# Kernel tuning notes

Hardware: AMD Instinct MI355X
Metric: run time of the kernel (lower is better)

## Reference

```python
import jax, jax.numpy as jnp
import numpy as np
from jax import lax

B, D, E, H, W = 256, 64, 16, 64, 64
PROJ, FC, NA = 512, 1024, 2

def _conv(x, w, pad):
    # x: [N,C,H,W], w: [O,I,kh,kw]
    return lax.conv_general_dilated(x, w, (1, 1), [(pad, pad), (pad, pad)],
                                    dimension_numbers=('NCHW', 'OIHW', 'NCHW'))

def _maxpool2(x):
    return lax.reduce_window(x, -jnp.inf, lax.max, (1, 1, 2, 2), (1, 1, 2, 2), 'VALID')

def _sample_conv(x, w, b):
    # per-sample conv with its own gathered expert weights: x [D,h,w], w [D,D,3,3]
    y = lax.conv_general_dilated(x[None], w, (1, 1), [(1, 1), (1, 1)],
                                 dimension_numbers=('NCHW', 'OIHW', 'NCHW'))[0]
    return y + b[:, None, None]

_expert_conv = jax.vmap(_sample_conv)  # batch of samples, each with its own kernel

def setup_inputs() -> dict:
    key = jax.random.key(0)
    ks = jax.random.split(key, 12)
    s = 0.05
    return {
        'image': jax.random.normal(ks[0], (B, 3, H, W), jnp.float32),
        'question': jax.random.randint(ks[1], (B, 8), 0, E),
        'stem_w0': jax.random.normal(ks[2], (D, 3, 3, 3), jnp.float32) * s,
        'stem_b0': jnp.zeros((D,), jnp.float32),
        'stem_w': jax.random.normal(ks[3], (3, D, D, 3, 3), jnp.float32) * s,
        'stem_b': jnp.zeros((3, D), jnp.float32),
        'exp_w1': jax.random.normal(ks[4], (E, D, D, 3, 3), jnp.float32) * s,
        'exp_b1': jnp.zeros((E, D), jnp.float32),
        'exp_w2': jax.random.normal(ks[5], (E, D, D, 3, 3), jnp.float32) * s,
        'exp_b2': jnp.zeros((E, D), jnp.float32),
        'proj_w': jax.random.normal(ks[6], (PROJ, D, 1, 1), jnp.float32) * s,
        'proj_b': jnp.zeros((PROJ,), jnp.float32),
        'fc1_w': jax.random.normal(ks[7], (FC, PROJ * 8 * 8), jnp.float32) * 0.01,
        'fc1_b': jnp.zeros((FC,), jnp.float32),
        'fc2_w': jax.random.normal(ks[8], (NA, FC), jnp.float32) * 0.01,
        'fc2_b': jnp.zeros((NA,), jnp.float32),
    }

def reference(image, question, stem_w0, stem_b0, stem_w, stem_b,
              exp_w1, exp_b1, exp_w2, exp_b2,
              proj_w, proj_b, fc1_w, fc1_b, fc2_w, fc2_b):
    # --- stem: 4 conv3x3 + ReLU, maxpool after layers 0 and 2 (64->32->16) ---
    h = jax.nn.relu(_conv(image, stem_w0, 1) + stem_b0[None, :, None, None])
    h = _maxpool2(h)
    h = jax.nn.relu(_conv(h, stem_w[0], 1) + stem_b[0][None, :, None, None])
    h = jax.nn.relu(_conv(h, stem_w[1], 1) + stem_b[1][None, :, None, None])
    h = _maxpool2(h)
    h = jax.nn.relu(_conv(h, stem_w[2], 1) + stem_b[2][None, :, None, None])
    # --- chain1 routing: cols (lhs=4, rel=5, rhs=7) each pick a ResidualBlock expert ---
    for col in (4, 5, 7):
        idx = question[:, col]                       # [B] expert ids
        w1, b1 = exp_w1[idx], exp_b1[idx]            # gather per-sample kernels
        w2, b2 = exp_w2[idx], exp_b2[idx]
        mid = jax.nn.relu(_expert_conv(h, w1, b1))   # conv1 + ReLU
        out = _expert_conv(mid, w2, b2)              # conv2 (no BN)
        h = jax.nn.relu(h + out)                     # residual + ReLU
    # --- classifier: 1x1 proj + ReLU, maxpool2, flatten, fc, fc ---
    c = jax.nn.relu(_conv(h, proj_w, 0) + proj_b[None, :, None, None])  # [B,512,16,16]
    c = _maxpool2(c)                                                     # [B,512,8,8]
    c = c.reshape(c.shape[0], -1)                                        # [B,32768]
    c = jax.nn.relu(c @ fc1_w.T + fc1_b)
    return c @ fc2_w.T + fc2_b                                           # [B,2]
```

## Files before the change

kernel.cpp:

```cpp
#include <hip/hip_runtime.h>
#include <cstddef>


typedef _Float16 half8 __attribute__((ext_vector_type(8)));
typedef _Float16 half4_t __attribute__((ext_vector_type(4)));
typedef float f32x4 __attribute__((ext_vector_type(4)));

#define LO_SCALE 2048.0f
#define LO_INV (1.0f / 2048.0f)

__global__ void wxform_k(const float* __restrict__ src, _Float16* __restrict__ dst,
                         int nlayers) {
    int id = blockIdx.x * 256 + threadIdx.x;
    if (id >= nlayers * 36864) return;
    int layer = id / 36864, idx = id % 36864;
    int j = idx & 7, l = (idx >> 3) & 63, nt = (idx >> 9) & 3;
    int icc = (idx >> 11) & 1, tap = idx >> 12;
    int kl = (l >> 4) * 8 + j, ic = icc * 32 + kl, oc = nt * 16 + (l & 15);
    float v = src[(size_t)layer * 36864 + (oc * 64 + ic) * 9 + tap];
    _Float16 hi = (_Float16)v;
    _Float16 lo = (_Float16)((v - (float)hi) * LO_SCALE);
    dst[(size_t)layer * 73728 + idx] = hi;
    dst[(size_t)layer * 73728 + 36864 + idx] = lo;
}

__global__ void pwxform_k(const float* __restrict__ src, _Float16* __restrict__ dst) {
    int id = blockIdx.x * 256 + threadIdx.x;
    if (id >= 32768) return;
    int j = id & 7, l = (id >> 3) & 63, icc = (id >> 9) & 1, nt = id >> 10;
    int kl = (l >> 4) * 8 + j, ic = icc * 32 + kl, oc = nt * 16 + (l & 15);
    float v = src[oc * 64 + ic];
    _Float16 hi = (_Float16)v;
    _Float16 lo = (_Float16)((v - (float)hi) * LO_SCALE);
    dst[id] = hi;
    dst[32768 + id] = lo;
}

__global__ void c1wx_k(const float* __restrict__ src, _Float16* __restrict__ dst) {
    int id = blockIdx.x * 256 + threadIdx.x;
    if (id >= 2048) return;
    int j = id & 7, l = (id >> 3) & 63, nt = id >> 9;
    int k = (l >> 4) * 8 + j, oc = nt * 16 + (l & 15);
    float v = 0.f;
    if (k < 27) {
        int ic = k / 9, tap = k % 9;
        v = src[(oc * 3 + ic) * 9 + tap];
    }
    _Float16 hi = (_Float16)v;
    _Float16 lo = (_Float16)((v - (float)hi) * LO_SCALE);
    dst[id] = hi;
    dst[2048 + id] = lo;
}

__global__ __launch_bounds__(256, 2)
void conv1m_k(const float* __restrict__ img, const _Float16* __restrict__ wf,
              const float* __restrict__ b0, _Float16* __restrict__ out) {
    const size_t NE1 = 16777216;
    int b = blockIdx.x, t = blockIdx.y;
    int ty0 = (t >> 2) * 8, tx0 = (t & 3) * 16;
    __shared__ float halo[3][10][18];
    __shared__ __align__(16) _Float16 lin[2 * 5120];

    int tid = threadIdx.x, lane = tid & 63, wv = tid >> 6;
    const float* imb = img + (size_t)b * 3 * 64 * 64;
    for (int i = tid; i < 540; i += 256) {
        int c = i / 180, rem = i % 180, r = rem / 18, cc = rem % 18;
        int gy = ty0 - 1 + r, gx = tx0 - 1 + cc;
        float v = 0.f;
        if (gy >= 0 && gy < 64 && gx >= 0 && gx < 64) v = imb[(c * 64 + gy) * 64 + gx];
        halo[c][r][cc] = v;
    }
    __syncthreads();
    for (int i = tid; i < 512; i += 256) {
        int r = i >> 2, j8 = (i & 3) * 8;
        int MT = r >> 4, am = r & 15;
        int Q = MT * 4 + (am >> 2), s = am & 3;
        int py = (Q >> 3) * 2 + (s >> 1), px = (Q & 7) * 2 + (s & 1);
        half8 vh, vl;
#pragma unroll
        for (int j = 0; j < 8; ++j) {
            int k = j8 + j;
            float v = 0.f;
            if (k < 27) {
                int ic = k / 9, tap = k % 9;
                v = halo[ic][py + tap / 3][px + tap % 3];
            }
            _Float16 h = (_Float16)v;
            vh[j] = h;
            vl[j] = (_Float16)((v - (float)h) * LO_SCALE);
        }
        *(half8*)&lin[r * 40 + j8] = vh;
        *(half8*)&lin[5120 + r * 40 + j8] = vl;
    }
    __syncthreads();

    int am = lane & 15, k0 = (lane >> 4) * 8;
    float bv[4];
#pragma unroll
    for (int nt = 0; nt < 4; ++nt) bv[nt] = b0[nt * 16 + (lane & 15)];

    half8 bh[4], bl[4];
#pragma unroll
    for (int nt = 0; nt < 4; ++nt) {
        const _Float16* wp = wf + ((size_t)nt * 64 + lane) * 8;
        bh[nt] = *(const half8*)wp;
        bl[nt] = *(const half8*)(wp + 2048);
    }

    f32x4 acc1[2][4] = {};
    f32x4 acc2[2][4] = {};
#pragma unroll
    for (int mt = 0; mt < 2; ++mt) {
        int MT = wv * 2 + mt;
        const _Float16* ap = &lin[(MT * 16 + am) * 40 + k0];
        half8 ahi = *(const half8*)ap;
        half8 alo = *(const half8*)(ap + 5120);
#pragma unroll
        for (int nt = 0; nt < 4; ++nt) {
            acc1[mt][nt] = __builtin_amdgcn_mfma_f32_16x16x32_f16(
                ahi, bh[nt], acc1[mt][nt], 0, 0, 0);
            acc2[mt][nt] = __builtin_amdgcn_mfma_f32_16x16x32_f16(
                ahi, bl[nt], acc2[mt][nt], 0, 0, 0);
            acc2[mt][nt] = __builtin_amdgcn_mfma_f32_16x16x32_f16(
                alo, bh[nt], acc2[mt][nt], 0, 0, 0);
        }
    }

    int cn = lane & 15, rq = lane >> 4;
#pragma unroll
    for (int mt = 0; mt < 2; ++mt) {
        int MT = wv * 2 + mt;
        int Q = MT * 4 + rq;
        int qy = Q >> 3, qx = Q & 7;
#pragma unroll
        for (int nt = 0; nt < 4; ++nt) {
            int oc = nt * 16 + cn;
            float vals[4];
#pragma unroll
            for (int r = 0; r < 4; ++r)
                vals[r] = acc1[mt][nt][r] + acc2[mt][nt][r] * LO_INV + bv[nt];
            float m = fmaxf(fmaxf(vals[0], vals[1]), fmaxf(vals[2], vals[3]));
            m = fmaxf(m, 0.f);
            int opy = (ty0 >> 1) + qy, opx = (tx0 >> 1) + qx;
            size_t o = (((size_t)b * 32 + opy) * 32 + opx) * 64 + oc;
            _Float16 h = (_Float16)m;
            out[o] = h;
            out[NE1 + o] = (_Float16)((m - (float)h) * LO_SCALE);
        }
    }
}

template <int S, bool POOL, bool RES>
__global__ __launch_bounds__(256, 2)
void convm_k(const _Float16* __restrict__ in, _Float16* __restrict__ out,
             const _Float16* __restrict__ wf, const float* __restrict__ bias,
             const _Float16* __restrict__ res, const int* __restrict__ question,
             int qcol) {
    constexpr size_t NEin = (size_t)S * S * 64 * 256;
    constexpr size_t NEout = POOL ? NEin / 4 : NEin;
    int b = blockIdx.x, t = blockIdx.y;
    constexpr int NTX = S / 16;
    int ty0 = (t / NTX) * 8, tx0 = (t % NTX) * 16;

    __shared__ __align__(16) _Float16 lds[2 * 7200];

    int tid = threadIdx.x, lane = tid & 63, wv = tid >> 6;
    const _Float16* wb = wf;
    const float* bb = bias;
    if (question) {
        int idx = question[b * 8 + qcol];
        wb += (size_t)idx * 73728;
        bb += idx * 64;
    }
    float bv[4];
#pragma unroll
    for (int nt = 0; nt < 4; ++nt) bv[nt] = bb[nt * 16 + (lane & 15)];

    f32x4 acc1[2][4] = {};
    f32x4 acc2[2][4] = {};

    int am = lane & 15;
    int k0 = (lane >> 4) * 8;

    for (int icc = 0; icc < 2; ++icc) {
        __syncthreads();
        for (int i = tid; i < 720; i += 256) {
            int pix = i >> 2, j8 = (i & 3) * 8;
            int hy = pix / 18, hx = pix % 18;
            int gy = ty0 + hy - 1, gx = tx0 + hx - 1;
            half8 vh = {}, vl = {};
            if (gy >= 0 && gy < S && gx >= 0 && gx < S) {
                size_t src = (((size_t)b * S + gy) * S + gx) * 64 + icc * 32 + j8;
                vh = *(const half8*)&in[src];
                vl = *(const half8*)&in[NEin + src];
            }
            *(half8*)&lds[pix * 40 + j8] = vh;
            *(half8*)&lds[7200 + pix * 40 + j8] = vl;
        }
        __syncthreads();

#pragma unroll
        for (int ky = 0; ky < 3; ++ky)
#pragma unroll
            for (int kx = 0; kx < 3; ++kx) {
                int tap = ky * 3 + kx;
                const _Float16* wp = wb + (tap * 2 + icc) * 2048 + lane * 8;
                half8 bhi[4], blo[4];
#pragma unroll
                for (int nt = 0; nt < 4; ++nt) {
                    bhi[nt] = *(const half8*)(wp + nt * 512);
                    blo[nt] = *(const half8*)(wp + nt * 512 + 36864);
                }
#pragma unroll
                for (int mt = 0; mt < 2; ++mt) {
                    int MT = wv * 2 + mt;
                    int Q = MT * 4 + (am >> 2), s = am & 3;
                    int py = (Q >> 3) * 2 + (s >> 1), px = (Q & 7) * 2 + (s & 1);
                    const _Float16* ap = &lds[((py + ky) * 18 + (px + kx)) * 40 + k0];
                    half8 ahi = *(const half8*)ap;
                    half8 alo = *(const half8*)(ap + 7200);
#pragma unroll
                    for (int nt = 0; nt < 4; ++nt) {
                        acc1[mt][nt] = __builtin_amdgcn_mfma_f32_16x16x32_f16(
                            ahi, bhi[nt], acc1[mt][nt], 0, 0, 0);
                        acc2[mt][nt] = __builtin_amdgcn_mfma_f32_16x16x32_f16(
                            ahi, blo[nt], acc2[mt][nt], 0, 0, 0);
                        acc2[mt][nt] = __builtin_amdgcn_mfma_f32_16x16x32_f16(
                            alo, bhi[nt], acc2[mt][nt], 0, 0, 0);
                    }
                }
            }
    }

    int cn = lane & 15, rq = lane >> 4;
#pragma unroll
    for (int mt = 0; mt < 2; ++mt) {
        int MT = wv * 2 + mt;
        int Q = MT * 4 + rq;
        int qy = Q >> 3, qx = Q & 7;
#pragma unroll
        for (int nt = 0; nt < 4; ++nt) {
            int oc = nt * 16 + cn;
            float vals[4];
#pragma unroll
            for (int r = 0; r < 4; ++r)
                vals[r] = acc1[mt][nt][r] + acc2[mt][nt][r] * LO_INV + bv[nt];
            if (POOL) {
                float m = fmaxf(fmaxf(vals[0], vals[1]), fmaxf(vals[2], vals[3]));
                m = fmaxf(m, 0.f);
                int opy = (ty0 >> 1) + qy, opx = (tx0 >> 1) + qx;
                size_t o = (((size_t)b * (S / 2) + opy) * (S / 2) + opx) * 64 + oc;
                _Float16 h = (_Float16)m;
                out[o] = h;
                out[NEout + o] = (_Float16)((m - (float)h) * LO_SCALE);
            } else {
#pragma unroll
                for (int r = 0; r < 4; ++r) {
                    int py = qy * 2 + (r >> 1), px = qx * 2 + (r & 1);
                    size_t o = (((size_t)b * S + (ty0 + py)) * S + (tx0 + px)) * 64 + oc;
                    float v = vals[r];
                    if (RES) v += (float)res[o] + (float)res[NEin + o] * LO_INV;
                    v = fmaxf(v, 0.f);
                    _Float16 h = (_Float16)v;
                    out[o] = h;
                    out[NEout + o] = (_Float16)((v - (float)h) * LO_SCALE);
                }
            }
        }
    }
}

__global__ __launch_bounds__(256)
void projm_k(const _Float16* __restrict__ in ,
             const _Float16* __restrict__ pw, const float* __restrict__ bias,
             _Float16* __restrict__ outh ) {
    const size_t NE2 = 4194304;
    int b = blockIdx.x;
    __shared__ float lt[64 * 65];
    int tid = threadIdx.x, lane = tid & 63, wv = tid >> 6;
    int row = lane & 15, cseg = lane >> 4;

    half8 ah[4][2], al[4][2];
#pragma unroll
    for (int mt = 0; mt < 4; ++mt) {
        int MT = wv * 4 + mt;
        int Q = MT * 4 + (row >> 2), s = row & 3;
        int y = (Q >> 3) * 2 + (s >> 1), x = (Q & 7) * 2 + (s & 1);
        size_t pb = ((size_t)b * 256 + y * 16 + x) * 64 + cseg * 8;
#pragma unroll
        for (int icc = 0; icc < 2; ++icc) {
            ah[mt][icc] = *(const half8*)&in[pb + icc * 32];
            al[mt][icc] = *(const half8*)&in[NE2 + pb + icc * 32];
        }
    }

    for (int ogl = 0; ogl < 4; ++ogl) {
        int og = blockIdx.y * 4 + ogl;
        half8 bh[4][2], bl[4][2];
#pragma unroll
        for (int ntl = 0; ntl < 4; ++ntl)
#pragma unroll
            for (int icc = 0; icc < 2; ++icc) {
                int nt = og * 4 + ntl;
                const _Float16* wp = pw + ((nt * 2 + icc) * 64 + lane) * 8;
                bh[ntl][icc] = *(const half8*)wp;
                bl[ntl][icc] = *(const half8*)(wp + 32768);
            }
        f32x4 a1[4][4] = {};
        f32x4 a2[4][4] = {};
#pragma unroll
        for (int icc = 0; icc < 2; ++icc)
#pragma unroll
            for (int mt = 0; mt < 4; ++mt)
#pragma unroll
                for (int ntl = 0; ntl < 4; ++ntl) {
                    a1[mt][ntl] = __builtin_amdgcn_mfma_f32_16x16x32_f16(
                        ah[mt][icc], bh[ntl][icc], a1[mt][ntl], 0, 0, 0);
                    a2[mt][ntl] = __builtin_amdgcn_mfma_f32_16x16x32_f16(
                        ah[mt][icc], bl[ntl][icc], a2[mt][ntl], 0, 0, 0);
                    a2[mt][ntl] = __builtin_amdgcn_mfma_f32_16x16x32_f16(
                        al[mt][icc], bh[ntl][icc], a2[mt][ntl], 0, 0, 0);
                }
        if (ogl) __syncthreads();
#pragma unroll
        for (int mt = 0; mt < 4; ++mt) {
            int Qg = (wv * 4 + mt) * 4 + (lane >> 4);
#pragma unroll
            for (int ntl = 0; ntl < 4; ++ntl) {
                float bvv = bias[og * 64 + ntl * 16 + (lane & 15)];
                float v0 = a1[mt][ntl][0] + a2[mt][ntl][0] * LO_INV + bvv;
                float v1 = a1[mt][ntl][1] + a2[mt][ntl][1] * LO_INV + bvv;
                float v2 = a1[mt][ntl][2] + a2[mt][ntl][2] * LO_INV + bvv;
                float v3 = a1[mt][ntl][3] + a2[mt][ntl][3] * LO_INV + bvv;
                float m = fmaxf(fmaxf(fmaxf(v0, v1), fmaxf(v2, v3)), 0.f);
                lt[(ntl * 16 + (lane & 15)) * 65 + Qg] = m;
            }
        }
        __syncthreads();
#pragma unroll
        for (int r = 0; r < 16; ++r) {
            int f = r * 256 + tid;
            int ol = f >> 6, q = f & 63;
            float v = lt[ol * 65 + q];
            _Float16 h = (_Float16)v;
            _Float16 l = (_Float16)((v - (float)h) * LO_SCALE);
            size_t o = (size_t)b * 32768 + og * 4096 + ol * 64 + q;
            outh[o] = h;
            outh[8388608 + o] = l;
        }
    }
}

__global__ __launch_bounds__(256)
void fc1m_k(const _Float16* __restrict__ Ahl ,
            const float* __restrict__ W,
            float* __restrict__ partial ) {
    int bid = blockIdx.x;
    int lid = (bid & 7) * 64 + (bid >> 3);
    int mt = lid & 1, nt = (lid >> 1) & 7, ks = lid >> 4;
    int m0 = mt * 128, n0 = nt * 128;
    const _Float16* Ab = Ahl + (size_t)m0 * 32768 + ks * 1024;
    const float* Wb = W + (size_t)n0 * 32768 + ks * 1024;

    __shared__ __align__(16) _Float16 lds[40960];

    int tid = threadIdx.x, lane = tid & 63, wv = tid >> 6;
    int wm = (wv & 1) * 64, wn = (wv >> 1) * 64;
    int koff = (lane >> 4) * 8, fr = lane & 15;

    f32x4 acc1[4][4] = {};
    f32x4 acc2[4][4] = {};

    int arow[2], ak8[2];
#pragma unroll
    for (int p = 0; p < 2; ++p) {
        int idx = p * 256 + tid;
        arow[p] = idx >> 2;
        ak8[p] = (idx & 3) * 8;
    }
    int wrow[4], wc4[4];
#pragma unroll
    for (int p = 0; p < 4; ++p) {
        int idx = p * 256 + tid;
        wrow[p] = idx >> 3;
        wc4[p] = (idx & 7) << 2;
    }

    half8 pa_h[2], pa_l[2];
    float4 rw[4];

#pragma unroll
    for (int p = 0; p < 2; ++p) {
        pa_h[p] = *(const half8*)&Ab[(size_t)arow[p] * 32768 + ak8[p]];
        pa_l[p] = *(const half8*)&Ab[8388608 + (size_t)arow[p] * 32768 + ak8[p]];
    }
#pragma unroll
    for (int p = 0; p < 4; ++p)
        rw[p] = *(const float4*)&Wb[(size_t)wrow[p] * 32768 + wc4[p]];
    {
        _Float16* b0p = lds;
#pragma unroll
        for (int p = 0; p < 2; ++p) {
            *(half8*)&b0p[arow[p] * 40 + ak8[p]] = pa_h[p];
            *(half8*)&b0p[5120 + arow[p] * 40 + ak8[p]] = pa_l[p];
        }
#pragma unroll
        for (int p = 0; p < 4; ++p) {
            float4 u = rw[p];
            _Float16 g0 = (_Float16)u.x, g1 = (_Float16)u.y;
            _Float16 g2 = (_Float16)u.z, g3 = (_Float16)u.w;
            half4_t gh = {g0, g1, g2, g3};
            half4_t gl = {(_Float16)((u.x - (float)g0) * LO_SCALE),
                          (_Float16)((u.y - (float)g1) * LO_SCALE),
                          (_Float16)((u.z - (float)g2) * LO_SCALE),
                          (_Float16)((u.w - (float)g3) * LO_SCALE)};
            *(half4_t*)&b0p[10240 + wrow[p] * 40 + wc4[p]] = gh;
            *(half4_t*)&b0p[15360 + wrow[p] * 40 + wc4[p]] = gl;
        }
    }
#pragma unroll
    for (int p = 0; p < 2; ++p) {
        pa_h[p] = *(const half8*)&Ab[(size_t)arow[p] * 32768 + 32 + ak8[p]];
        pa_l[p] = *(const half8*)&Ab[8388608 + (size_t)arow[p] * 32768 + 32 + ak8[p]];
    }
#pragma unroll
    for (int p = 0; p < 4; ++p)
        rw[p] = *(const float4*)&Wb[(size_t)wrow[p] * 32768 + 32 + wc4[p]];
    __syncthreads();

    for (int kt = 0; kt < 32; ++kt) {
        _Float16* cur = lds + (kt & 1) * 20480;
        _Float16* nxt = lds + ((kt + 1) & 1) * 20480;
        if (kt < 31) {
#pragma unroll
            for (int p = 0; p < 2; ++p) {
                *(half8*)&nxt[arow[p] * 40 + ak8[p]] = pa_h[p];
                *(half8*)&nxt[5120 + arow[p] * 40 + ak8[p]] = pa_l[p];
            }
#pragma unroll
            for (int p = 0; p < 4; ++p) {
                float4 u = rw[p];
                _Float16 g0 = (_Float16)u.x, g1 = (_Float16)u.y;
                _Float16 g2 = (_Float16)u.z, g3 = (_Float16)u.w;
                half4_t gh = {g0, g1, g2, g3};
                half4_t gl = {(_Float16)((u.x - (float)g0) * LO_SCALE),
                              (_Float16)((u.y - (float)g1) * LO_SCALE),
                              (_Float16)((u.z - (float)g2) * LO_SCALE),
                              (_Float16)((u.w - (float)g3) * LO_SCALE)};
                *(half4_t*)&nxt[10240 + wrow[p] * 40 + wc4[p]] = gh;
                *(half4_t*)&nxt[15360 + wrow[p] * 40 + wc4[p]] = gl;
            }
            if (kt < 30) {
                int kb = (kt + 2) * 32;
#pragma unroll
                for (int p = 0; p < 2; ++p) {
                    pa_h[p] = *(const half8*)&Ab[(size_t)arow[p] * 32768 + kb + ak8[p]];
                    pa_l[p] = *(const half8*)&Ab[8388608 + (size_t)arow[p] * 32768 + kb + ak8[p]];
                }
#pragma unroll
                for (int p = 0; p < 4; ++p)
                    rw[p] = *(const float4*)&Wb[(size_t)wrow[p] * 32768 + kb + wc4[p]];
            }
        }
        half8 bh[4], bl[4];
#pragma unroll
        for (int nf = 0; nf < 4; ++nf) {
            int r = wn + nf * 16 + fr;
            bh[nf] = *(const half8*)&cur[10240 + r * 40 + koff];
            bl[nf] = *(const half8*)&cur[15360 + r * 40 + koff];
        }
#pragma unroll
        for (int mf = 0; mf < 4; ++mf) {
            int r = wm + mf * 16 + fr;
            half8 ah = *(const half8*)&cur[r * 40 + koff];
            half8 al = *(const half8*)&cur[5120 + r * 40 + koff];
#pragma unroll
            for (int nf = 0; nf < 4; ++nf) {
                acc1[mf][nf] = __builtin_amdgcn_mfma_f32_16x16x32_f16(
                    ah, bh[nf], acc1[mf][nf], 0, 0, 0);
                acc2[mf][nf] = __builtin_amdgcn_mfma_f32_16x16x32_f16(
                    ah, bl[nf], acc2[mf][nf], 0, 0, 0);
                acc2[mf][nf] = __builtin_amdgcn_mfma_f32_16x16x32_f16(
                    al, bh[nf], acc2[mf][nf], 0, 0, 0);
            }
        }
        __syncthreads();
    }

    int rq = lane >> 4, cn = lane & 15;
    float* pb = partial + (size_t)ks * 262144;
#pragma unroll
    for (int mf = 0; mf < 4; ++mf)
#pragma unroll
        for (int nf = 0; nf < 4; ++nf) {
            int n = n0 + wn + nf * 16 + cn;
#pragma unroll
            for (int r = 0; r < 4; ++r) {
                int m = m0 + wm + mf * 16 + rq * 4 + r;
                pb[(size_t)m * 1024 + n] = acc1[mf][nf][r] + acc2[mf][nf][r] * LO_INV;
            }
        }
}

__global__ __launch_bounds__(256)
void fc1red_k(const float* __restrict__ partial, const float* __restrict__ b1,
              float* __restrict__ fc1o_t ) {
    int m = blockIdx.x;
    int n0 = threadIdx.x * 4;
    float4 s = {0.f, 0.f, 0.f, 0.f};
    for (int ks = 0; ks < 32; ++ks) {
        float4 v = *(const float4*)&partial[((size_t)ks * 256 + m) * 1024 + n0];
        s.x += v.x; s.y += v.y; s.z += v.z; s.w += v.w;
    }
    fc1o_t[(size_t)(n0 + 0) * 256 + m] = fmaxf(s.x + b1[n0 + 0], 0.f);
    fc1o_t[(size_t)(n0 + 1) * 256 + m] = fmaxf(s.y + b1[n0 + 1], 0.f);
    fc1o_t[(size_t)(n0 + 2) * 256 + m] = fmaxf(s.z + b1[n0 + 2], 0.f);
    fc1o_t[(size_t)(n0 + 3) * 256 + m] = fmaxf(s.w + b1[n0 + 3], 0.f);
}

__global__ __launch_bounds__(256)
void fc2a_k(const float* __restrict__ a_t, const float* __restrict__ W2,
            float* __restrict__ p2) {
    int n2 = blockIdx.x, ks = blockIdx.y;
    int m = threadIdx.x;
    float acc = 0.f;
    for (int k = ks * 256; k < ks * 256 + 256; ++k)
        acc = fmaf(a_t[(size_t)k * 256 + m], W2[n2 * 1024 + k], acc);
    p2[((size_t)n2 * 4 + ks) * 256 + m] = acc;
}

__global__ __launch_bounds__(512)
void fc2b_k(const float* __restrict__ p2, const float* __restrict__ b2,
            float* __restrict__ out) {
    int i = threadIdx.x;
    int m = i >> 1, n2 = i & 1;
    float s = b2[n2];
#pragma unroll
    for (int ks = 0; ks < 4; ++ks) s += p2[((size_t)n2 * 4 + ks) * 256 + m];
    out[m * 2 + n2] = s;
}

extern "C" void kernel_launch(void* const* d_in, const int* in_sizes, int n_in,
                              void* d_out, int out_size, void* d_ws, size_t ws_size,
                              hipStream_t stream) {
    const float* image   = (const float*)d_in[0];
    const int*   question= (const int*)d_in[1];
    const float* stem_w0 = (const float*)d_in[2];
    const float* stem_b0 = (const float*)d_in[3];
    const float* stem_w  = (const float*)d_in[4];
    const float* stem_b  = (const float*)d_in[5];
    const float* exp_w1  = (const float*)d_in[6];
    const float* exp_b1  = (const float*)d_in[7];
    const float* exp_w2  = (const float*)d_in[8];
    const float* exp_b2  = (const float*)d_in[9];
    const float* proj_w  = (const float*)d_in[10];
    const float* proj_b  = (const float*)d_in[11];
    const float* fc1_w   = (const float*)d_in[12];
    const float* fc1_b   = (const float*)d_in[13];
    const float* fc2_w   = (const float*)d_in[14];
    const float* fc2_b   = (const float*)d_in[15];
    (void)in_sizes; (void)n_in; (void)out_size; (void)ws_size;

    float* ws = (float*)d_ws;
    const size_t A = 16777216, P2N = 4194304;
    float* wtr   = ws + 2 * A + P2N;
    _Float16* c1wF = (_Float16*)wtr;
    _Float16* pwF = (_Float16*)(wtr + 2048);
    float* pfc2  = wtr + 2048 + 32768;
    _Float16* f16b = (_Float16*)(wtr + 36864);
    _Float16* stemtF = f16b;
    _Float16* e1tF   = f16b + 3 * 73728;
    _Float16* e2tF   = e1tF + 16 * 73728;
    _Float16* p1h  = (_Float16*)ws;
    _Float16* h2h  = (_Float16*)(ws + A);
    _Float16* p2h  = (_Float16*)(ws + 2 * A);
    _Float16* hAh  = (_Float16*)ws;
    _Float16* hBh  = (_Float16*)(ws + P2N);
    _Float16* hCh  = (_Float16*)(ws + 2 * P2N);
    _Float16* pool3h = (_Float16*)(ws + A);
    float* fc1o  = ws + A + 8388608;
    float* fc1p  = ws;

    c1wx_k<<<8, 256, 0, stream>>>(stem_w0, c1wF);
    pwxform_k<<<128, 256, 0, stream>>>(proj_w, pwF);
    wxform_k<<<(3 * 36864 + 255) / 256, 256, 0, stream>>>(stem_w, stemtF, 3);
    wxform_k<<<(16 * 36864 + 255) / 256, 256, 0, stream>>>(exp_w1, e1tF, 16);
    wxform_k<<<(16 * 36864 + 255) / 256, 256, 0, stream>>>(exp_w2, e2tF, 16);

    conv1m_k<<<dim3(256, 32), 256, 0, stream>>>(image, c1wF, stem_b0, p1h);
    convm_k<32, false, false><<<dim3(256, 8), 256, 0, stream>>>(
        p1h, h2h, stemtF, stem_b, nullptr, nullptr, 0);
    convm_k<32, true, false><<<dim3(256, 8), 256, 0, stream>>>(
        h2h, p2h, stemtF + 73728, stem_b + 64, nullptr, nullptr, 0);
    convm_k<16, false, false><<<dim3(256, 2), 256, 0, stream>>>(
        p2h, hAh, stemtF + 2 * 73728, stem_b + 128, nullptr, nullptr, 0);

    const int cols[3] = {4, 5, 7};
    _Float16* hin = hAh;
    _Float16* hmid = hBh;
    _Float16* hout = hCh;
    for (int r = 0; r < 3; ++r) {
        convm_k<16, false, false><<<dim3(256, 2), 256, 0, stream>>>(
            hin, hmid, e1tF, exp_b1, nullptr, question, cols[r]);
        convm_k<16, false, true><<<dim3(256, 2), 256, 0, stream>>>(
            hmid, hout, e2tF, exp_b2, hin, question, cols[r]);
        _Float16* tp = hin; hin = hout; hout = hmid; hmid = tp;
    }

    projm_k<<<dim3(256, 2), 256, 0, stream>>>(hin, pwF, proj_b, pool3h);
    fc1m_k<<<512, 256, 0, stream>>>(pool3h, fc1_w, fc1p);
    fc1red_k<<<256, 256, 0, stream>>>(fc1p, fc1_b, fc1o);
    fc2a_k<<<dim3(2, 4), 256, 0, stream>>>(fc1o, fc2_w, pfc2);
    fc2b_k<<<1, 512, 0, stream>>>(pfc2, fc2_b, (float*)d_out);
}
```

Before: 437.1 us.

## Single-buffer fc1 LDS tiles with padded stride to cut shared memory

Replaces the double-buffered LDS staging in the fc1 split-K GEMM with a single buffer, adding a barrier after each tile store. The row stride changes from 40 to 42 halves, which alters the bank mapping. The goal is to roughly halve LDS use so more blocks can be resident per CU. In exchange, the LDS store of tile k+1 no longer overlaps the MFMA work on tile k. The odd-aligned 84-byte row stride also breaks 16-byte alignment for the half8 LDS reads, which may split or slow those reads.

```diff
diff --git a/kernel.cpp b/kernel.cpp
--- a/kernel.cpp
+++ b/kernel.cpp
@@ -362,7 +362,9 @@
     const _Float16* Ab = Ahl + (size_t)m0 * 32768 + ks * 1024;
     const float* Wb = W + (size_t)n0 * 32768 + ks * 1024;
 
-    __shared__ __align__(16) _Float16 lds[40960];
+    __shared__ __align__(16) _Float16 lds[21504];
+    _Float16* sa = lds;
+    _Float16* sb = lds + 10752;
 
     int tid = threadIdx.x, lane = tid & 63, wv = tid >> 6;
     int wm = (wv & 1) * 64, wn = (wv >> 1) * 64;
@@ -388,7 +390,6 @@
 
     half8 pa_h[2], pa_l[2];
     float4 rw[4];
-
 #pragma unroll
     for (int p = 0; p < 2; ++p) {
         pa_h[p] = *(const half8*)&Ab[(size_t)arow[p] * 32768 + ak8[p]];
@@ -397,12 +398,12 @@
 #pragma unroll
     for (int p = 0; p < 4; ++p)
         rw[p] = *(const float4*)&Wb[(size_t)wrow[p] * 32768 + wc4[p]];
-    {
-        _Float16* b0p = lds;
+
+    for (int kt = 0; kt < 32; ++kt) {
 #pragma unroll
         for (int p = 0; p < 2; ++p) {
-            *(half8*)&b0p[arow[p] * 40 + ak8[p]] = pa_h[p];
-            *(half8*)&b0p[5120 + arow[p] * 40 + ak8[p]] = pa_l[p];
+            *(half8*)&sa[arow[p] * 42 + ak8[p]] = pa_h[p];
+            *(half8*)&sa[5376 + arow[p] * 42 + ak8[p]] = pa_l[p];
         }
 #pragma unroll
         for (int p = 0; p < 4; ++p) {
@@ -414,66 +415,33 @@
                           (_Float16)((u.y - (float)g1) * LO_SCALE),
                           (_Float16)((u.z - (float)g2) * LO_SCALE),
                           (_Float16)((u.w - (float)g3) * LO_SCALE)};
-            *(half4_t*)&b0p[10240 + wrow[p] * 40 + wc4[p]] = gh;
-            *(half4_t*)&b0p[15360 + wrow[p] * 40 + wc4[p]] = gl;
-        }
-    }
-#pragma unroll
-    for (int p = 0; p < 2; ++p) {
-        pa_h[p] = *(const half8*)&Ab[(size_t)arow[p] * 32768 + 32 + ak8[p]];
-        pa_l[p] = *(const half8*)&Ab[8388608 + (size_t)arow[p] * 32768 + 32 + ak8[p]];
-    }
-#pragma unroll
-    for (int p = 0; p < 4; ++p)
-        rw[p] = *(const float4*)&Wb[(size_t)wrow[p] * 32768 + 32 + wc4[p]];
-    __syncthreads();
-
-    for (int kt = 0; kt < 32; ++kt) {
-        _Float16* cur = lds + (kt & 1) * 20480;
-        _Float16* nxt = lds + ((kt + 1) & 1) * 20480;
+            *(half4_t*)&sb[wrow[p] * 42 + wc4[p]] = gh;
+            *(half4_t*)&sb[5376 + wrow[p] * 42 + wc4[p]] = gl;
+        }
+        __syncthreads();
         if (kt < 31) {
+            int kb = (kt + 1) * 32;
 #pragma unroll
             for (int p = 0; p < 2; ++p) {
-                *(half8*)&nxt[arow[p] * 40 + ak8[p]] = pa_h[p];
-                *(half8*)&nxt[5120 + arow[p] * 40 + ak8[p]] = pa_l[p];
-            }
-#pragma unroll
-            for (int p = 0; p < 4; ++p) {
-                float4 u = rw[p];
-                _Float16 g0 = (_Float16)u.x, g1 = (_Float16)u.y;
-                _Float16 g2 = (_Float16)u.z, g3 = (_Float16)u.w;
-                half4_t gh = {g0, g1, g2, g3};
-                half4_t gl = {(_Float16)((u.x - (float)g0) * LO_SCALE),
-                              (_Float16)((u.y - (float)g1) * LO_SCALE),
-                              (_Float16)((u.z - (float)g2) * LO_SCALE),
-                              (_Float16)((u.w - (float)g3) * LO_SCALE)};
-                *(half4_t*)&nxt[10240 + wrow[p] * 40 + wc4[p]] = gh;
-                *(half4_t*)&nxt[15360 + wrow[p] * 40 + wc4[p]] = gl;
-            }
-            if (kt < 30) {
-                int kb = (kt + 2) * 32;
-#pragma unroll
-                for (int p = 0; p < 2; ++p) {
-                    pa_h[p] = *(const half8*)&Ab[(size_t)arow[p] * 32768 + kb + ak8[p]];
-                    pa_l[p] = *(const half8*)&Ab[8388608 + (size_t)arow[p] * 32768 + kb + ak8[p]];
-                }
-#pragma unroll
-                for (int p = 0; p < 4; ++p)
-                    rw[p] = *(const float4*)&Wb[(size_t)wrow[p] * 32768 + kb + wc4[p]];
-            }
+                pa_h[p] = *(const half8*)&Ab[(size_t)arow[p] * 32768 + kb + ak8[p]];
+                pa_l[p] = *(const half8*)&Ab[8388608 + (size_t)arow[p] * 32768 + kb + ak8[p]];
+            }
+#pragma unroll
+            for (int p = 0; p < 4; ++p)
+                rw[p] = *(const float4*)&Wb[(size_t)wrow[p] * 32768 + kb + wc4[p]];
         }
         half8 bh[4], bl[4];
 #pragma unroll
         for (int nf = 0; nf < 4; ++nf) {
             int r = wn + nf * 16 + fr;
-            bh[nf] = *(const half8*)&cur[10240 + r * 40 + koff];
-            bl[nf] = *(const half8*)&cur[15360 + r * 40 + koff];
+            bh[nf] = *(const half8*)&sb[r * 42 + koff];
+            bl[nf] = *(const half8*)&sb[5376 + r * 42 + koff];
         }
 #pragma unroll
         for (int mf = 0; mf < 4; ++mf) {
             int r = wm + mf * 16 + fr;
-            half8 ah = *(const half8*)&cur[r * 40 + koff];
-            half8 al = *(const half8*)&cur[5120 + r * 40 + koff];
+            half8 ah = *(const half8*)&sa[r * 42 + koff];
+            half8 al = *(const half8*)&sa[5376 + r * 42 + koff];
 #pragma unroll
             for (int nf = 0; nf < 4; ++nf) {
                 acc1[mf][nf] = __builtin_amdgcn_mfma_f32_16x16x32_f16(
```

After: 608.5 us. +39.2%, slower.
